# Optimization experiments

Measured on AMD Instinct MI355X. Metric: run time of the kernel, lower is better.

The kernel has to match this reference:

```python
import jax, jax.numpy as jnp
import numpy as np

D_MODEL = 1024
NUM_HEADS = 16
HEAD_DIM = D_MODEL // NUM_HEADS
D_FF = 4 * D_MODEL


def setup_inputs() -> dict:
    key = jax.random.key(0)
    ks = jax.random.split(key, 16)
    s = 0.02
    inp = {
        "x": jax.random.normal(ks[0], (2, 2048, D_MODEL), dtype=jnp.float32),
        "w_q": jax.random.normal(ks[1], (D_MODEL, D_MODEL), dtype=jnp.float32) * s,
        "b_q": jnp.zeros((D_MODEL,), jnp.float32),
        "w_k": jax.random.normal(ks[2], (D_MODEL, D_MODEL), dtype=jnp.float32) * s,
        "b_k": jnp.zeros((D_MODEL,), jnp.float32),
        "w_v": jax.random.normal(ks[3], (D_MODEL, D_MODEL), dtype=jnp.float32) * s,
        "b_v": jnp.zeros((D_MODEL,), jnp.float32),
        "w_o": jax.random.normal(ks[4], (D_MODEL, D_MODEL), dtype=jnp.float32) * s,
        "b_o": jnp.zeros((D_MODEL,), jnp.float32),
        "w_ff1": jax.random.normal(ks[5], (D_MODEL, D_FF), dtype=jnp.float32) * s,
        "b_ff1": jnp.zeros((D_FF,), jnp.float32),
        "w_ff2": jax.random.normal(ks[6], (D_FF, D_MODEL), dtype=jnp.float32) * s,
        "b_ff2": jnp.zeros((D_MODEL,), jnp.float32),
        "ln1_g": jnp.ones((D_MODEL,), jnp.float32),
        "ln1_b": jnp.zeros((D_MODEL,), jnp.float32),
        "ln2_g": jnp.ones((D_MODEL,), jnp.float32),
        "ln2_b": jnp.zeros((D_MODEL,), jnp.float32),
    }
    return inp


def layer_norm(x, g, b, eps=1e-5):
    mu = jnp.mean(x, axis=-1, keepdims=True)
    var = jnp.var(x, axis=-1, keepdims=True)
    return (x - mu) * jax.lax.rsqrt(var + eps) * g + b


def encoder_block(x, w_q, b_q, w_k, b_k, w_v, b_v, w_o, b_o,
                  w_ff1, b_ff1, w_ff2, b_ff2, ln1_g, ln1_b, ln2_g, ln2_b):
    B, S, _ = x.shape
    # QKV projections -> [B, H, S, hd]
    def proj(w, b):
        return (x @ w + b).reshape(B, S, NUM_HEADS, HEAD_DIM).transpose(0, 2, 1, 3)
    q, k, v = proj(w_q, b_q), proj(w_k, b_k), proj(w_v, b_v)
    scale = 1.0 / jnp.sqrt(jnp.float32(HEAD_DIM))
    score = jnp.einsum('bhqd,bhkd->bhqk', q, k) * scale  # [B,H,S,S]
    attn = jax.nn.softmax(score, axis=-1)
    ctx = jnp.einsum('bhqk,bhkd->bhqd', attn, v)
    ctx = ctx.transpose(0, 2, 1, 3).reshape(B, S, D_MODEL)
    attn_out = ctx @ w_o + b_o
    # AddNorm1 (dropout = identity at inference)
    h = layer_norm(x + attn_out, ln1_g, ln1_b)
    # FFN
    ff = jax.nn.relu(h @ w_ff1 + b_ff1) @ w_ff2 + b_ff2
    # AddNorm2
    return layer_norm(h + ff, ln2_g, ln2_b)


def reference(x, w_q, b_q, w_k, b_k, w_v, b_v, w_o, b_o,
              w_ff1, b_ff1, w_ff2, b_ff2, ln1_g, ln1_b, ln2_g, ln2_b):
    return encoder_block(x, w_q, b_q, w_k, b_k, w_v, b_v, w_o, b_o,
                         w_ff1, b_ff1, w_ff2, b_ff2, ln1_g, ln1_b, ln2_g, ln2_b)
```

## Files before the change

### kernel.cpp

```cpp
#include <hip/hip_runtime.h>
#include <hip/hip_bf16.h>

typedef __attribute__((ext_vector_type(8))) short short8;
typedef __attribute__((ext_vector_type(4))) float f32x4;
typedef unsigned short u16;
typedef unsigned int u32;

constexpr float CSC = 0.18033688f;

__device__ __forceinline__ u16 f2bf(float f) {
    __hip_bfloat16 h = __float2bfloat16(f);
    return __builtin_bit_cast(u16, h);
}
__device__ __forceinline__ u32 packtrunc(float a, float b) {
    const u32 ua = __builtin_bit_cast(u32, a);
    const u32 ub = __builtin_bit_cast(u32, b);
    return (ua >> 16) | (ub & 0xffff0000u);
}

#if __has_builtin(__builtin_amdgcn_exp2f)
#define EXP2(x) __builtin_amdgcn_exp2f(x)
#else
#define EXP2(x) exp2f(x)
#endif

#define GLD16(g, l) __builtin_amdgcn_global_load_lds( \
    (const __attribute__((address_space(1))) void*)(g), \
    (__attribute__((address_space(3))) void*)(l), 16, 0, 0)

__global__ __launch_bounds__(256) void prep_kernel(
    const float* __restrict__ x, u16* __restrict__ xb,
    const float* __restrict__ w_q, const float* __restrict__ w_k,
    const float* __restrict__ w_v, const float* __restrict__ w_o,
    const float* __restrict__ w_ff1, const float* __restrict__ w_ff2,
    u16* __restrict__ wqkvT, u16* __restrict__ woT,
    u16* __restrict__ wf1T, u16* __restrict__ wf2T,
    const float* __restrict__ bq, const float* __restrict__ bk,
    const float* __restrict__ bv, float* __restrict__ bout)
{
    __shared__ float tile[32][33];
    int id = blockIdx.x;
    const int t = threadIdx.x;
    if (id < 1024) {
        const int i = id * 256 + t;
        float4 v = ((const float4*)x)[i];
        *(ushort4*)(xb + 4 * (size_t)i) =
            make_ushort4(f2bf(v.x), f2bf(v.y), f2bf(v.z), f2bf(v.w));
        return;
    }
    id -= 1024;
    const float* src; u16* dst; int R, C, bx, by;
    if (id < 4096) {
        const int w = id >> 10, tt = id & 1023;
        src = w == 0 ? w_q : (w == 1 ? w_k : (w == 2 ? w_v : w_o));
        dst = w < 3 ? wqkvT + (size_t)w * 1024 * 1024 : woT;
        R = 1024; C = 1024; bx = (tt & 31) * 32; by = (tt >> 5) * 32;
    } else if (id < 8192) {
        const int tt = id - 4096;
        src = w_ff1; dst = wf1T;
        R = 1024; C = 4096; bx = (tt & 127) * 32; by = (tt >> 7) * 32;
    } else if (id < 12288) {
        const int tt = id - 8192;
        src = w_ff2; dst = wf2T;
        R = 4096; C = 1024; bx = (tt & 31) * 32; by = (tt >> 5) * 32;
    } else {
        for (int i = t; i < 1024; i += 256) {
            bout[i] = bq[i]; bout[1024 + i] = bk[i]; bout[2048 + i] = bv[i];
        }
        return;
    }
    const int tx = t & 31, ty = t >> 5;
    #pragma unroll
    for (int i = 0; i < 32; i += 8)
        tile[ty + i][tx] = src[(size_t)(by + ty + i) * C + bx + tx];
    __syncthreads();
    #pragma unroll
    for (int i = 0; i < 32; i += 8)
        dst[(size_t)(bx + ty + i) * R + by + tx] = f2bf(tile[tx][ty + i]);
}

template<bool RELU, int TM, bool QKV>
__global__ __launch_bounds__(256, 2) void gemm_bt(
    const u16* __restrict__ A, const u16* __restrict__ BT,
    const float* __restrict__ bias, u16* __restrict__ C,
    u16* __restrict__ VT, int M, int N, int K)
{
    __shared__ __align__(16) u16 As[TM * 32];
    __shared__ __align__(16) u16 Bs[128 * 32];
    constexpr int MW = TM / 32;
    constexpr int NCH_A = TM * 4;
    constexpr int NITER = (NCH_A + 512) / 256;
    const int t = threadIdx.x;
    const int wave = t >> 6, lane = t & 63;
    const int quad = lane >> 4, l16 = lane & 15;
    const int wm = (wave >> 1) * (TM / 2), wn = (wave & 1) * 64;
    const size_t rowA = (size_t)blockIdx.x * TM;
    const size_t rowB = (size_t)blockIdx.y * 128;

    f32x4 acc[MW][4] = {};

    for (int k0 = 0; k0 < K; k0 += 32) {
        __syncthreads();
        #pragma unroll
        for (int j = 0; j < NITER; ++j) {
            const int cb = j * 256 + wave * 64;
            const int c = cb + lane;
            if (j * 256 < NCH_A) {
                const int m = c >> 2, kq = c & 3;
                GLD16(A + (rowA + m) * K + k0 + kq * 8, As + cb * 8);
            } else {
                const int c2 = c - NCH_A;
                const int m = c2 >> 2, kq = c2 & 3;
                GLD16(BT + (rowB + m) * K + k0 + kq * 8, Bs + (cb - NCH_A) * 8);
            }
        }
        __syncthreads();
        short8 af[MW], bf[4];
        #pragma unroll
        for (int i = 0; i < MW; ++i)
            af[i] = *(const short8*)(As + (wm + i * 16 + l16) * 32 + quad * 8);
        #pragma unroll
        for (int j = 0; j < 4; ++j)
            bf[j] = *(const short8*)(Bs + (wn + j * 16 + l16) * 32 + quad * 8);
        #pragma unroll
        for (int i = 0; i < MW; ++i)
            #pragma unroll
            for (int j = 0; j < 4; ++j)
                acc[i][j] = __builtin_amdgcn_mfma_f32_16x16x32_bf16(
                    af[i], bf[j], acc[i][j], 0, 0, 0);
    }

    if (QKV && (int)blockIdx.y >= 16) {
        #pragma unroll
        for (int i = 0; i < MW; ++i) {
            #pragma unroll
            for (int j = 0; j < 4; ++j) {
                const int vcol = (int)rowB + wn + j * 16 + l16 - 2048;
                const int hh = vcol >> 6, dd = vcol & 63;
                const float bv = bias[vcol + 2048];
                const int row0 = (int)rowA + wm + i * 16 + quad * 4;
                const int bb = row0 >> 11, ss = row0 & 2047;
                ushort4 pk;
                pk.x = f2bf(acc[i][j][0] + bv);
                pk.y = f2bf(acc[i][j][1] + bv);
                pk.z = f2bf(acc[i][j][2] + bv);
                pk.w = f2bf(acc[i][j][3] + bv);
                *(ushort4*)(VT + ((size_t)(bb * 16 + hh) * 64 + dd) * 2048 + ss) = pk;
            }
        }
    } else {
        const float sc = (QKV && (int)blockIdx.y < 8) ? CSC : 1.0f;
        #pragma unroll
        for (int i = 0; i < MW; ++i) {
            #pragma unroll
            for (int j = 0; j < 4; ++j) {
                const int col = (int)rowB + wn + j * 16 + l16;
                const float bv = bias[col];
                #pragma unroll
                for (int r = 0; r < 4; ++r) {
                    const int row = (int)rowA + wm + i * 16 + quad * 4 + r;
                    float v = (acc[i][j][r] + bv) * sc;
                    if (RELU) v = fmaxf(v, 0.f);
                    C[(size_t)row * N + col] = f2bf(v);
                }
            }
        }
    }
}

template<int TM>
__global__ __launch_bounds__(256, 2) void gemm_bt_sk(
    const u16* __restrict__ A, const u16* __restrict__ BT,
    float* __restrict__ Cp0, float* __restrict__ Cp1,
    int M, int N, int K, int Kspl)
{
    __shared__ __align__(16) u16 As[TM * 32];
    __shared__ __align__(16) u16 Bs[128 * 32];
    constexpr int MW = TM / 32;
    constexpr int NCH_A = TM * 4;
    constexpr int NITER = (NCH_A + 512) / 256;
    const int t = threadIdx.x;
    const int wave = t >> 6, lane = t & 63;
    const int quad = lane >> 4, l16 = lane & 15;
    const int wm = (wave >> 1) * (TM / 2), wn = (wave & 1) * 64;
    const size_t rowA = (size_t)blockIdx.x * TM;
    const size_t rowB = (size_t)blockIdx.y * 128;
    const int kbeg = blockIdx.z * Kspl;

    f32x4 acc[MW][4] = {};

    for (int k0 = kbeg; k0 < kbeg + Kspl; k0 += 32) {
        __syncthreads();
        #pragma unroll
        for (int j = 0; j < NITER; ++j) {
            const int cb = j * 256 + wave * 64;
            const int c = cb + lane;
            if (j * 256 < NCH_A) {
                const int m = c >> 2, kq = c & 3;
                GLD16(A + (rowA + m) * K + k0 + kq * 8, As + cb * 8);
            } else {
                const int c2 = c - NCH_A;
                const int m = c2 >> 2, kq = c2 & 3;
                GLD16(BT + (rowB + m) * K + k0 + kq * 8, Bs + (cb - NCH_A) * 8);
            }
        }
        __syncthreads();
        short8 af[MW], bf[4];
        #pragma unroll
        for (int i = 0; i < MW; ++i)
            af[i] = *(const short8*)(As + (wm + i * 16 + l16) * 32 + quad * 8);
        #pragma unroll
        for (int j = 0; j < 4; ++j)
            bf[j] = *(const short8*)(Bs + (wn + j * 16 + l16) * 32 + quad * 8);
        #pragma unroll
        for (int i = 0; i < MW; ++i)
            #pragma unroll
            for (int j = 0; j < 4; ++j)
                acc[i][j] = __builtin_amdgcn_mfma_f32_16x16x32_bf16(
                    af[i], bf[j], acc[i][j], 0, 0, 0);
    }

    float* out = blockIdx.z == 0 ? Cp0 : Cp1;
    #pragma unroll
    for (int i = 0; i < MW; ++i)
        #pragma unroll
        for (int j = 0; j < 4; ++j) {
            const int col = (int)rowB + wn + j * 16 + l16;
            #pragma unroll
            for (int r = 0; r < 4; ++r) {
                const int row = (int)rowA + wm + i * 16 + quad * 4 + r;
                out[(size_t)row * N + col] = acc[i][j][r];
            }
        }
}

__global__ __launch_bounds__(256, 4) void flash_attn(
    const u16* __restrict__ qkv, const u16* __restrict__ vt,
    u16* __restrict__ ctx)
{
    __shared__ __align__(16) u16 Ks[64 * 64];
    __shared__ __align__(16) u16 Vs[64 * 64];
    __shared__ __align__(16) u16 Ps[4 * 16 * 72];
    const int t = threadIdx.x;
    const int wave = t >> 6, lane = t & 63;
    const int quad = lane >> 4, l16 = lane & 15;
    const int h = blockIdx.y, b = blockIdx.z;
    const int q0 = blockIdx.x * 64 + wave * 16;
    const size_t rowbase = (size_t)b * 2048;
    const u16* kb = qkv + rowbase * 3072 + 1024 + h * 64;
    const u16* vb = vt + (size_t)(b * 16 + h) * 64 * 2048;
    u16* pw = Ps + wave * 16 * 72;

    short8 aq[2];
    #pragma unroll
    for (int ksb = 0; ksb < 2; ++ksb)
        aq[ksb] = *(const short8*)(qkv +
            (rowbase + q0 + l16) * 3072 + h * 64 + ksb * 32 + quad * 8);

    f32x4 o[4] = {};
    f32x4 lp4 = {};

    for (int kv0 = 0; kv0 < 2048; kv0 += 64) {
        __syncthreads();
        #pragma unroll
        for (int j = 0; j < 2; ++j) {
            const int cb = j * 256 + wave * 64;
            const int slot = cb + lane;
            const int row = slot >> 3;
            const int kq = (slot & 7) ^ (row & 7);
            GLD16(kb + (size_t)(kv0 + row) * 3072 + kq * 8, Ks + cb * 8);
            GLD16(vb + (size_t)row * 2048 + kv0 + kq * 8, Vs + cb * 8);
        }
        __syncthreads();

        f32x4 st[4] = {};
        #pragma unroll
        for (int ksb = 0; ksb < 2; ++ksb) {
            #pragma unroll
            for (int mt = 0; mt < 4; ++mt) {
                const short8 ak = *(const short8*)(Ks +
                    ((mt * 16 + l16) * 8 + ((ksb * 4 + quad) ^ (l16 & 7))) * 8);
                st[mt] = __builtin_amdgcn_mfma_f32_16x16x32_bf16(
                    ak, aq[ksb], st[mt], 0, 0, 0);
            }
        }

        #pragma unroll
        for (int mt = 0; mt < 4; ++mt) {
            const float p0 = EXP2(st[mt][0]);
            const float p1 = EXP2(st[mt][1]);
            const float p2 = EXP2(st[mt][2]);
            const float p3 = EXP2(st[mt][3]);
            lp4 = lp4 + (f32x4){p0, p1, p2, p3};
            *(uint2*)(pw + l16 * 72 + mt * 16 + quad * 4) =
                make_uint2(packtrunc(p0, p1), packtrunc(p2, p3));
        }

        #pragma unroll
        for (int ksb = 0; ksb < 2; ++ksb) {
            const short8 ap = *(const short8*)(pw + l16 * 72 + ksb * 32 + quad * 8);
            #pragma unroll
            for (int dt = 0; dt < 4; ++dt) {
                const short8 bv = *(const short8*)(Vs +
                    ((dt * 16 + l16) * 8 + ((ksb * 4 + quad) ^ (l16 & 7))) * 8);
                o[dt] = __builtin_amdgcn_mfma_f32_16x16x32_bf16(
                    ap, bv, o[dt], 0, 0, 0);
            }
        }
    }

    float lp = (lp4[0] + lp4[1]) + (lp4[2] + lp4[3]);
    lp += __shfl_xor(lp, 16, 64);
    lp += __shfl_xor(lp, 32, 64);

    #pragma unroll
    for (int r = 0; r < 4; ++r) {
        const float inv = 1.0f / __shfl(lp, quad * 4 + r, 64);
        const size_t row = rowbase + q0 + quad * 4 + r;
        #pragma unroll
        for (int dt = 0; dt < 4; ++dt)
            ctx[row * 1024 + h * 64 + dt * 16 + l16] = f2bf(o[dt][r] * inv);
    }
}

__global__ __launch_bounds__(256) void add_norm_p_kernel(
    const float* __restrict__ a, const float* __restrict__ p0,
    const float* __restrict__ p1, const float* __restrict__ cb,
    const float* __restrict__ g, const float* __restrict__ bbv,
    float* __restrict__ out32, u16* __restrict__ out16)
{
    __shared__ float red[8];
    const int row = blockIdx.x, t = threadIdx.x;
    const int wave = t >> 6, lane = t & 63;
    const size_t base = (size_t)row * 1024 + t * 4;
    const int c = t * 4;
    float4 av = *(const float4*)(a + base);
    float4 q0 = *(const float4*)(p0 + base);
    float4 q1 = *(const float4*)(p1 + base);
    float4 cv = *(const float4*)(cb + c);
    float v0 = av.x + q0.x + q1.x + cv.x;
    float v1 = av.y + q0.y + q1.y + cv.y;
    float v2 = av.z + q0.z + q1.z + cv.z;
    float v3 = av.w + q0.w + q1.w + cv.w;
    float sum = v0 + v1 + v2 + v3;
    float sq  = v0 * v0 + v1 * v1 + v2 * v2 + v3 * v3;
    #pragma unroll
    for (int msk = 1; msk < 64; msk <<= 1) {
        sum += __shfl_xor(sum, msk, 64);
        sq  += __shfl_xor(sq,  msk, 64);
    }
    if (lane == 0) { red[wave] = sum; red[wave + 4] = sq; }
    __syncthreads();
    sum = red[0] + red[1] + red[2] + red[3];
    sq  = red[4] + red[5] + red[6] + red[7];
    const float mu  = sum * (1.f / 1024.f);
    const float var = sq * (1.f / 1024.f) - mu * mu;
    const float rstd = rsqrtf(var + 1e-5f);
    float o0 = (v0 - mu) * rstd * g[c + 0] + bbv[c + 0];
    float o1 = (v1 - mu) * rstd * g[c + 1] + bbv[c + 1];
    float o2 = (v2 - mu) * rstd * g[c + 2] + bbv[c + 2];
    float o3 = (v3 - mu) * rstd * g[c + 3] + bbv[c + 3];
    *(float4*)(out32 + base) = make_float4(o0, o1, o2, o3);
    if (out16)
        *(ushort4*)(out16 + base) = make_ushort4(f2bf(o0), f2bf(o1), f2bf(o2), f2bf(o3));
}

extern "C" void kernel_launch(void* const* d_in, const int* in_sizes, int n_in,
                              void* d_out, int out_size, void* d_ws, size_t ws_size,
                              hipStream_t stream)
{
    const float* x     = (const float*)d_in[0];
    const float* w_q   = (const float*)d_in[1];
    const float* b_q   = (const float*)d_in[2];
    const float* w_k   = (const float*)d_in[3];
    const float* b_k   = (const float*)d_in[4];
    const float* w_v   = (const float*)d_in[5];
    const float* b_v   = (const float*)d_in[6];
    const float* w_o   = (const float*)d_in[7];
    const float* b_o   = (const float*)d_in[8];
    const float* w_ff1 = (const float*)d_in[9];
    const float* b_ff1 = (const float*)d_in[10];
    const float* w_ff2 = (const float*)d_in[11];
    const float* b_ff2 = (const float*)d_in[12];
    const float* ln1_g = (const float*)d_in[13];
    const float* ln1_b = (const float*)d_in[14];
    const float* ln2_g = (const float*)d_in[15];
    const float* ln2_b = (const float*)d_in[16];

    char* ws = (char*)d_ws;
    u16*   xb    = (u16*)(ws);
    u16*   wqkvT = (u16*)(ws + (8ull  << 20));
    u16*   woT   = (u16*)(ws + (14ull << 20));
    u16*   wf1T  = (u16*)(ws + (16ull << 20));
    u16*   wf2T  = (u16*)(ws + (24ull << 20));
    float* bqkv  = (float*)(ws + (32ull << 20));
    u16*   qkv   = (u16*)(ws + (33ull << 20));
    u16*   ctx   = (u16*)(ws + (57ull << 20));
    float* h32   = (float*)(ws + (65ull << 20));
    u16*   hb    = (u16*)(ws + (81ull << 20));
    u16*   ff    = (u16*)(ws + (89ull << 20));
    u16*   vt    = (u16*)(ws + (121ull << 20));
    float* pO0   = (float*)(ws + (33ull << 20));
    float* pO1   = (float*)(ws + (121ull << 20));
    float* pF0   = (float*)(ws + (33ull << 20));
    float* pF1   = (float*)(ws + (49ull << 20));

    prep_kernel<<<13313, 256, 0, stream>>>(
        x, xb, w_q, w_k, w_v, w_o, w_ff1, w_ff2,
        wqkvT, woT, wf1T, wf2T, b_q, b_k, b_v, bqkv);

    gemm_bt<false, 128, true ><<<dim3(32, 24), 256, 0, stream>>>(
        xb, wqkvT, bqkv, qkv, vt, 4096, 3072, 1024);
    flash_attn<<<dim3(32, 16, 2), 256, 0, stream>>>(qkv, vt, ctx);
    gemm_bt_sk<128><<<dim3(32, 8, 2), 256, 0, stream>>>(
        ctx, woT, pO0, pO1, 4096, 1024, 1024, 512);
    add_norm_p_kernel<<<4096, 256, 0, stream>>>(
        x, pO0, pO1, b_o, ln1_g, ln1_b, h32, hb);
    gemm_bt<true, 128, false><<<dim3(32, 32), 256, 0, stream>>>(
        hb, wf1T, b_ff1, ff, nullptr, 4096, 4096, 1024);
    gemm_bt_sk<128><<<dim3(32, 8, 2), 256, 0, stream>>>(
        ff, wf2T, pF0, pF1, 4096, 1024, 4096, 2048);
    add_norm_p_kernel<<<4096, 256, 0, stream>>>(
        h32, pF0, pF1, b_ff2, ln2_g, ln2_b, (float*)d_out, nullptr);
}
```

Measured before the change: 352.9 us.

## Double query rows per wave in flash attention to reuse K/V tiles

Each wave in the attention kernel now handles 32 query rows instead of 16, so one block covers 128 queries and the grid halves. The K and V fragments read from shared memory are reused across two query sub-tiles, cutting LDS reads and global K/V reloads per query. In exchange it uses more registers, so the occupancy hint drops to 2 and only 512 blocks are launched. The GEMM kernels' launch-bounds occupancy hint is also raised from 2 to 3, which may force register spilling.

Result: no change. 349.2 us (-1.1%).

```diff
diff --git a/kernel.cpp b/kernel.cpp
--- a/kernel.cpp
+++ b/kernel.cpp
@@ -80,7 +80,7 @@
 }
 
 template<bool RELU, int TM, bool QKV>
-__global__ __launch_bounds__(256, 2) void gemm_bt(
+__global__ __launch_bounds__(256, 3) void gemm_bt(
     const u16* __restrict__ A, const u16* __restrict__ BT,
     const float* __restrict__ bias, u16* __restrict__ C,
     u16* __restrict__ VT, int M, int N, int K)
@@ -169,7 +169,7 @@
 }
 
 template<int TM>
-__global__ __launch_bounds__(256, 2) void gemm_bt_sk(
+__global__ __launch_bounds__(256, 3) void gemm_bt_sk(
     const u16* __restrict__ A, const u16* __restrict__ BT,
     float* __restrict__ Cp0, float* __restrict__ Cp1,
     int M, int N, int K, int Kspl)
@@ -234,31 +234,33 @@
         }
 }
 
-__global__ __launch_bounds__(256, 4) void flash_attn(
+__global__ __launch_bounds__(256, 2) void flash_attn(
     const u16* __restrict__ qkv, const u16* __restrict__ vt,
     u16* __restrict__ ctx)
 {
     __shared__ __align__(16) u16 Ks[64 * 64];
     __shared__ __align__(16) u16 Vs[64 * 64];
-    __shared__ __align__(16) u16 Ps[4 * 16 * 72];
+    __shared__ __align__(16) u16 Ps[4 * 32 * 72];
     const int t = threadIdx.x;
     const int wave = t >> 6, lane = t & 63;
     const int quad = lane >> 4, l16 = lane & 15;
     const int h = blockIdx.y, b = blockIdx.z;
-    const int q0 = blockIdx.x * 64 + wave * 16;
+    const int q0 = blockIdx.x * 128 + wave * 32;
     const size_t rowbase = (size_t)b * 2048;
     const u16* kb = qkv + rowbase * 3072 + 1024 + h * 64;
     const u16* vb = vt + (size_t)(b * 16 + h) * 64 * 2048;
-    u16* pw = Ps + wave * 16 * 72;
-
-    short8 aq[2];
-    #pragma unroll
-    for (int ksb = 0; ksb < 2; ++ksb)
-        aq[ksb] = *(const short8*)(qkv +
-            (rowbase + q0 + l16) * 3072 + h * 64 + ksb * 32 + quad * 8);
-
-    f32x4 o[4] = {};
-    f32x4 lp4 = {};
+    u16* pw = Ps + wave * 32 * 72;
+
+    short8 aq[2][2];
+    #pragma unroll
+    for (int m2 = 0; m2 < 2; ++m2)
+        #pragma unroll
+        for (int ksb = 0; ksb < 2; ++ksb)
+            aq[m2][ksb] = *(const short8*)(qkv +
+                (rowbase + q0 + m2 * 16 + l16) * 3072 + h * 64 + ksb * 32 + quad * 8);
+
+    f32x4 o[2][4] = {};
+    f32x4 lp4[2] = {};
 
     for (int kv0 = 0; kv0 < 2048; kv0 += 64) {
         __syncthreads();
@@ -273,53 +275,68 @@
         }
         __syncthreads();
 
-        f32x4 st[4] = {};
+        f32x4 st[2][4] = {};
         #pragma unroll
         for (int ksb = 0; ksb < 2; ++ksb) {
+            short8 ak[4];
+            #pragma unroll
+            for (int mt = 0; mt < 4; ++mt)
+                ak[mt] = *(const short8*)(Ks +
+                    ((mt * 16 + l16) * 8 + ((ksb * 4 + quad) ^ (l16 & 7))) * 8);
+            #pragma unroll
+            for (int m2 = 0; m2 < 2; ++m2)
+                #pragma unroll
+                for (int mt = 0; mt < 4; ++mt)
+                    st[m2][mt] = __builtin_amdgcn_mfma_f32_16x16x32_bf16(
+                        ak[mt], aq[m2][ksb], st[m2][mt], 0, 0, 0);
+        }
+
+        #pragma unroll
+        for (int m2 = 0; m2 < 2; ++m2) {
             #pragma unroll
             for (int mt = 0; mt < 4; ++mt) {
-                const short8 ak = *(const short8*)(Ks +
-                    ((mt * 16 + l16) * 8 + ((ksb * 4 + quad) ^ (l16 & 7))) * 8);
-                st[mt] = __builtin_amdgcn_mfma_f32_16x16x32_bf16(
-                    ak, aq[ksb], st[mt], 0, 0, 0);
-            }
-        }
-
-        #pragma unroll
-        for (int mt = 0; mt < 4; ++mt) {
-            const float p0 = EXP2(st[mt][0]);
-            const float p1 = EXP2(st[mt][1]);
-            const float p2 = EXP2(st[mt][2]);
-            const float p3 = EXP2(st[mt][3]);
-            lp4 = lp4 + (f32x4){p0, p1, p2, p3};
-            *(uint2*)(pw + l16 * 72 + mt * 16 + quad * 4) =
-                make_uint2(packtrunc(p0, p1), packtrunc(p2, p3));
+                const float p0 = EXP2(st[m2][mt][0]);
+                const float p1 = EXP2(st[m2][mt][1]);
+                const float p2 = EXP2(st[m2][mt][2]);
+                const float p3 = EXP2(st[m2][mt][3]);
+                lp4[m2] = lp4[m2] + (f32x4){p0, p1, p2, p3};
+                *(uint2*)(pw + (m2 * 16 + l16) * 72 + mt * 16 + quad * 4) =
+                    make_uint2(packtrunc(p0, p1), packtrunc(p2, p3));
+            }
         }
 
         #pragma unroll
         for (int ksb = 0; ksb < 2; ++ksb) {
-            const short8 ap = *(const short8*)(pw + l16 * 72 + ksb * 32 + quad * 8);
-            #pragma unroll
-            for (int dt = 0; dt < 4; ++dt) {
-                const short8 bv = *(const short8*)(Vs +
+            short8 bv[4];
+            #pragma unroll
+            for (int dt = 0; dt < 4; ++dt)
+                bv[dt] = *(const short8*)(Vs +
                     ((dt * 16 + l16) * 8 + ((ksb * 4 + quad) ^ (l16 & 7))) * 8);
-                o[dt] = __builtin_amdgcn_mfma_f32_16x16x32_bf16(
-                    ap, bv, o[dt], 0, 0, 0);
-            }
-        }
-    }
-
-    float lp = (lp4[0] + lp4[1]) + (lp4[2] + lp4[3]);
-    lp += __shfl_xor(lp, 16, 64);
-    lp += __shfl_xor(lp, 32, 64);
-
-    #pragma unroll
-    for (int r = 0; r < 4; ++r) {
-        const float inv = 1.0f / __shfl(lp, quad * 4 + r, 64);
-        const size_t row = rowbase + q0 + quad * 4 + r;
-        #pragma unroll
-        for (int dt = 0; dt < 4; ++dt)
-            ctx[row * 1024 + h * 64 + dt * 16 + l16] = f2bf(o[dt][r] * inv);
+            #pragma unroll
+            for (int m2 = 0; m2 < 2; ++m2) {
+                const short8 ap = *(const short8*)(pw +
+                    (m2 * 16 + l16) * 72 + ksb * 32 + quad * 8);
+                #pragma unroll
+                for (int dt = 0; dt < 4; ++dt)
+                    o[m2][dt] = __builtin_amdgcn_mfma_f32_16x16x32_bf16(
+                        ap, bv[dt], o[m2][dt], 0, 0, 0);
+            }
+        }
+    }
+
+    #pragma unroll
+    for (int m2 = 0; m2 < 2; ++m2) {
+        float lp = (lp4[m2][0] + lp4[m2][1]) + (lp4[m2][2] + lp4[m2][3]);
+        lp += __shfl_xor(lp, 16, 64);
+        lp += __shfl_xor(lp, 32, 64);
+        #pragma unroll
+        for (int r = 0; r < 4; ++r) {
+            const float inv = 1.0f / __shfl(lp, quad * 4 + r, 64);
+            const size_t row = rowbase + q0 + m2 * 16 + quad * 4 + r;
+            #pragma unroll
+            for (int dt = 0; dt < 4; ++dt)
+                ctx[row * 1024 + h * 64 + dt * 16 + l16] = f2bf(o[m2][dt][r] * inv);
+        }
     }
 }
 
@@ -411,7 +428,7 @@
 
     gemm_bt<false, 128, true ><<<dim3(32, 24), 256, 0, stream>>>(
         xb, wqkvT, bqkv, qkv, vt, 4096, 3072, 1024);
-    flash_attn<<<dim3(32, 16, 2), 256, 0, stream>>>(qkv, vt, ctx);
+    flash_attn<<<dim3(16, 16, 2), 256, 0, stream>>>(qkv, vt, ctx);
     gemm_bt_sk<128><<<dim3(32, 8, 2), 256, 0, stream>>>(
         ctx, woT, pO0, pO1, 4096, 1024, 1024, 512);
     add_norm_p_kernel<<<4096, 256, 0, stream>>>(
```
